# Performance work log

Measured on AMD Instinct MI355X. Metric: run time of the kernel, lower is better.

The kernel has to match this reference:

```python
import jax, jax.numpy as jnp
import numpy as np

EPS = 1e-5
SLOPE = 0.2
DIMS = [128, 32, 64, 32, 16, 8, 4, 2]  # widths before final Linear(2,1)


def _layernorm(h, g, b):
    m = jnp.mean(h, axis=-1, keepdims=True)
    v = jnp.mean(jnp.square(h - m), axis=-1, keepdims=True)
    return (h - m) * jax.lax.rsqrt(v + EPS) * g + b


def setup_inputs() -> dict:
    key = jax.random.key(0)
    ks = jax.random.split(key, 2 * len(DIMS) + 2)
    inp = {"x": jax.random.normal(ks[0], (524288, DIMS[0]), dtype=jnp.float32)}
    # 7 bias-free Linears, each followed by LayerNorm(gamma, beta)
    for i in range(7):
        din, dout = DIMS[i], DIMS[i + 1]
        inp[f"W{i+1}"] = jax.random.normal(ks[2 * i + 1], (din, dout), dtype=jnp.float32) / np.sqrt(din)
        inp[f"g{i+1}"] = jnp.ones((dout,), dtype=jnp.float32)
        inp[f"bt{i+1}"] = jnp.zeros((dout,), dtype=jnp.float32)
    # final Linear(2 -> 1) with bias
    inp["W8"] = jax.random.normal(ks[-1], (2, 1), dtype=jnp.float32) / np.sqrt(2.0)
    inp["b8"] = jnp.zeros((1,), dtype=jnp.float32)
    return inp


def reference(x, W1, g1, bt1, W2, g2, bt2, W3, g3, bt3, W4, g4, bt4,
              W5, g5, bt5, W6, g6, bt6, W7, g7, bt7, W8, b8):
    Ws = [W1, W2, W3, W4, W5, W6, W7]
    gs = [g1, g2, g3, g4, g5, g6, g7]
    bs = [bt1, bt2, bt3, bt4, bt5, bt6, bt7]
    h = x
    for W, g, b in zip(Ws, gs, bs):
        h = jnp.dot(h, W)                 # Linear, bias=False
        h = _layernorm(h, g, b)           # LayerNorm
        h = jnp.where(h > 0, h, SLOPE * h)  # LeakyReLU(0.2)
    return jnp.dot(h, W8) + b8            # final Linear(2, 1)
```

## Files before the change

kernel.cpp:

```cpp
#include <hip/hip_runtime.h>

#define EPS 1e-5f
#define SLOPE 0.2f

typedef float v2f __attribute__((ext_vector_type(2)));

__device__ __forceinline__ v2f pkfma(float s, v2f w, v2f a) {
  v2f sv = {s, s};
  return __builtin_elementwise_fma(sv, w, a);
}

template<int N2>
__device__ __forceinline__ void ln_lrelu_pk(v2f* h, const float* __restrict__ g,
                                            const float* __restrict__ b) {
  const v2f* g2 = reinterpret_cast<const v2f*>(g);
  const v2f* b2 = reinterpret_cast<const v2f*>(b);
  const float invN = 1.0f / (2 * N2);
  float m, vv;
  if constexpr (N2 >= 2) {
    v2f s0 = {0.f, 0.f}, s1 = {0.f, 0.f};
#pragma unroll
    for (int j = 0; j < N2; j += 2) { s0 += h[j]; s1 += h[j + 1]; }
    v2f st = s0 + s1;
    m = (st.x + st.y) * invN;
    v2f q0 = {0.f, 0.f}, q1 = {0.f, 0.f};
#pragma unroll
    for (int j = 0; j < N2; j += 2) {
      v2f d0 = h[j] - m, d1 = h[j + 1] - m;
      q0 = __builtin_elementwise_fma(d0, d0, q0);
      q1 = __builtin_elementwise_fma(d1, d1, q1);
    }
    v2f qt = q0 + q1;
    vv = (qt.x + qt.y) * invN;
  } else {
    m = (h[0].x + h[0].y) * 0.5f;
    float dx = h[0].x - m, dy = h[0].y - m;
    vv = (dx * dx + dy * dy) * 0.5f;
  }
  const float rs = rsqrtf(vv + EPS);
#pragma unroll
  for (int j = 0; j < N2; ++j) {
    v2f t = (h[j] - m) * rs * g2[j] + b2[j];
    h[j] = __builtin_elementwise_max(t, SLOPE * t);
  }
}

template<int DIN, int DOUT2>
__device__ __forceinline__ void linear_pk(const v2f* hin, v2f* hout,
                                          const float* __restrict__ W) {
#pragma unroll
  for (int j = 0; j < DOUT2; ++j) hout[j] = (v2f){0.f, 0.f};
#pragma unroll
  for (int k = 0; k < DIN; ++k) {
    float hk = (k & 1) ? hin[k >> 1].y : hin[k >> 1].x;
    const v2f* wr = reinterpret_cast<const v2f*>(W + k * (DOUT2 * 2));
#pragma unroll
    for (int j = 0; j < DOUT2; ++j) hout[j] = pkfma(hk, wr[j], hout[j]);
  }
}

__global__ __launch_bounds__(256) void disc_fused(
    const float* __restrict__ x,
    const float* __restrict__ W1, const float* __restrict__ g1, const float* __restrict__ b1,
    const float* __restrict__ W2, const float* __restrict__ g2, const float* __restrict__ b2,
    const float* __restrict__ W3, const float* __restrict__ g3, const float* __restrict__ b3,
    const float* __restrict__ W4, const float* __restrict__ g4, const float* __restrict__ b4,
    const float* __restrict__ W5, const float* __restrict__ g5, const float* __restrict__ b5,
    const float* __restrict__ W6, const float* __restrict__ g6, const float* __restrict__ b6,
    const float* __restrict__ W7, const float* __restrict__ g7, const float* __restrict__ b7,
    const float* __restrict__ W8, const float* __restrict__ b8,
    float* __restrict__ out, int nrows) {
  const long row = (long)blockIdx.x * 256 + threadIdx.x;
  if (row >= (long)nrows) return;

  const float4* __restrict__ xr4 = reinterpret_cast<const float4*>(x) + row * 32;
  v2f h1[16];
#pragma unroll
  for (int j = 0; j < 16; ++j) h1[j] = (v2f){0.f, 0.f};

#pragma unroll 1
  for (int cc = 0; cc < 4; ++cc) {
    float4 bv[8];
#pragma unroll
    for (int q = 0; q < 8; ++q) bv[q] = xr4[cc * 8 + q];
#pragma unroll
    for (int q = 0; q < 8; ++q) {
#pragma unroll
      for (int kk = 0; kk < 4; ++kk) {
        float xk = (kk == 0) ? bv[q].x : (kk == 1) ? bv[q].y
                 : (kk == 2) ? bv[q].z : bv[q].w;
        const v2f* wr =
            reinterpret_cast<const v2f*>(W1 + (cc * 32 + q * 4 + kk) * 32);
#pragma unroll
        for (int j = 0; j < 16; ++j) h1[j] = pkfma(xk, wr[j], h1[j]);
      }
    }
  }
  ln_lrelu_pk<16>(h1, g1, b1);

  const v2f* W2v = reinterpret_cast<const v2f*>(W2);

  float sum2 = 0.f, sq2 = 0.f;
#pragma unroll 1
  for (int jb = 0; jb < 16; ++jb) {
    v2f a01 = {0.f, 0.f}, a23 = {0.f, 0.f};
#pragma unroll
    for (int k = 0; k < 32; ++k) {
      float hk = (k & 1) ? h1[k >> 1].y : h1[k >> 1].x;
      a01 = pkfma(hk, W2v[k * 32 + jb * 2], a01);
      a23 = pkfma(hk, W2v[k * 32 + jb * 2 + 1], a23);
    }
    sum2 += (a01.x + a01.y) + (a23.x + a23.y);
    sq2 = fmaf(a01.x, a01.x, sq2); sq2 = fmaf(a01.y, a01.y, sq2);
    sq2 = fmaf(a23.x, a23.x, sq2); sq2 = fmaf(a23.y, a23.y, sq2);
  }
  const float m2 = sum2 * (1.0f / 64.0f);
  const float v2 = fmaf(-m2, m2, sq2 * (1.0f / 64.0f));
  const float rs2 = rsqrtf(v2 + EPS);

  v2f h3[16];
#pragma unroll
  for (int i = 0; i < 16; ++i) h3[i] = (v2f){0.f, 0.f};
#pragma unroll 1
  for (int jb = 0; jb < 16; ++jb) {
    v2f a01 = {0.f, 0.f}, a23 = {0.f, 0.f};
#pragma unroll
    for (int k = 0; k < 32; ++k) {
      float hk = (k & 1) ? h1[k >> 1].y : h1[k >> 1].x;
      a01 = pkfma(hk, W2v[k * 32 + jb * 2], a01);
      a23 = pkfma(hk, W2v[k * 32 + jb * 2 + 1], a23);
    }
#pragma unroll
    for (int u = 0; u < 4; ++u) {
      float a = (u == 0) ? a01.x : (u == 1) ? a01.y : (u == 2) ? a23.x : a23.y;
      int j = jb * 4 + u;
      float y = (a - m2) * rs2 * g2[j] + b2[j];
      y = fmaxf(y, SLOPE * y);
      const v2f* wr3 = reinterpret_cast<const v2f*>(W3 + j * 32);
#pragma unroll
      for (int i = 0; i < 16; ++i) h3[i] = pkfma(y, wr3[i], h3[i]);
    }
  }
  ln_lrelu_pk<16>(h3, g3, b3);

  v2f h4[8]; linear_pk<32, 8>(h3, h4, W4); ln_lrelu_pk<8>(h4, g4, b4);
  v2f h5[4]; linear_pk<16, 4>(h4, h5, W5); ln_lrelu_pk<4>(h5, g5, b5);
  v2f h6[2]; linear_pk<8, 2>(h5, h6, W6);  ln_lrelu_pk<2>(h6, g6, b6);
  v2f h7[1]; linear_pk<4, 1>(h6, h7, W7);  ln_lrelu_pk<1>(h7, g7, b7);

  out[row] = fmaf(h7[0].y, W8[1], fmaf(h7[0].x, W8[0], b8[0]));
}

extern "C" void kernel_launch(void* const* d_in, const int* in_sizes, int n_in,
                              void* d_out, int out_size, void* d_ws, size_t ws_size,
                              hipStream_t stream) {
  const float* x  = (const float*)d_in[0];
  const float* W1 = (const float*)d_in[1];
  const float* g1 = (const float*)d_in[2];
  const float* b1 = (const float*)d_in[3];
  const float* W2 = (const float*)d_in[4];
  const float* g2 = (const float*)d_in[5];
  const float* b2 = (const float*)d_in[6];
  const float* W3 = (const float*)d_in[7];
  const float* g3 = (const float*)d_in[8];
  const float* b3 = (const float*)d_in[9];
  const float* W4 = (const float*)d_in[10];
  const float* g4 = (const float*)d_in[11];
  const float* b4 = (const float*)d_in[12];
  const float* W5 = (const float*)d_in[13];
  const float* g5 = (const float*)d_in[14];
  const float* b5 = (const float*)d_in[15];
  const float* W6 = (const float*)d_in[16];
  const float* g6 = (const float*)d_in[17];
  const float* b6 = (const float*)d_in[18];
  const float* W7 = (const float*)d_in[19];
  const float* g7 = (const float*)d_in[20];
  const float* b7 = (const float*)d_in[21];
  const float* W8 = (const float*)d_in[22];
  const float* b8 = (const float*)d_in[23];
  float* out = (float*)d_out;

  const int nrows = in_sizes[0] / 128;
  const int grid = (nrows + 255) / 256;
  hipLaunchKernelGGL(disc_fused, dim3(grid), dim3(256), 0, stream,
                     x, W1, g1, b1, W2, g2, b2, W3, g3, b3, W4, g4, b4,
                     W5, g5, b5, W6, g6, b6, W7, g7, b7, W8, b8, out, nrows);
}
```

Before: 151.9 us.

## Process two rows per thread to amortize weight loads across rows

Each thread now computes two consecutive rows, sharing every weight load between two sets of packed FMAs across all layers, and the grid is halved. A dummy 44KB shared-memory array caps occupancy so the doubled register footprint fits without spilling. The intent is to cut weight-load and instruction overhead per row. The cost is higher register pressure, fewer resident waves to hide memory latency, and less coalesced x reads because rows are strided by two per thread.

```diff
diff --git a/kernel.cpp b/kernel.cpp
--- a/kernel.cpp
+++ b/kernel.cpp
@@ -11,51 +11,73 @@
 }
 
 template<int N2>
-__device__ __forceinline__ void ln_lrelu_pk(v2f* h, const float* __restrict__ g,
-                                            const float* __restrict__ b) {
+__device__ __forceinline__ void ln_lrelu_pk2(v2f* __restrict__ ha, v2f* __restrict__ hb,
+                                             const float* __restrict__ g,
+                                             const float* __restrict__ b) {
   const v2f* g2 = reinterpret_cast<const v2f*>(g);
   const v2f* b2 = reinterpret_cast<const v2f*>(b);
   const float invN = 1.0f / (2 * N2);
-  float m, vv;
+  float ma, mb, va, vb;
   if constexpr (N2 >= 2) {
-    v2f s0 = {0.f, 0.f}, s1 = {0.f, 0.f};
-#pragma unroll
-    for (int j = 0; j < N2; j += 2) { s0 += h[j]; s1 += h[j + 1]; }
-    v2f st = s0 + s1;
-    m = (st.x + st.y) * invN;
-    v2f q0 = {0.f, 0.f}, q1 = {0.f, 0.f};
+    v2f sa0 = {0.f, 0.f}, sa1 = {0.f, 0.f}, sb0 = {0.f, 0.f}, sb1 = {0.f, 0.f};
 #pragma unroll
     for (int j = 0; j < N2; j += 2) {
-      v2f d0 = h[j] - m, d1 = h[j + 1] - m;
-      q0 = __builtin_elementwise_fma(d0, d0, q0);
-      q1 = __builtin_elementwise_fma(d1, d1, q1);
-    }
-    v2f qt = q0 + q1;
-    vv = (qt.x + qt.y) * invN;
+      sa0 += ha[j]; sa1 += ha[j + 1];
+      sb0 += hb[j]; sb1 += hb[j + 1];
+    }
+    v2f sat = sa0 + sa1, sbt = sb0 + sb1;
+    ma = (sat.x + sat.y) * invN;
+    mb = (sbt.x + sbt.y) * invN;
+    v2f qa0 = {0.f, 0.f}, qa1 = {0.f, 0.f}, qb0 = {0.f, 0.f}, qb1 = {0.f, 0.f};
+#pragma unroll
+    for (int j = 0; j < N2; j += 2) {
+      v2f da0 = ha[j] - ma, da1 = ha[j + 1] - ma;
+      v2f db0 = hb[j] - mb, db1 = hb[j + 1] - mb;
+      qa0 = __builtin_elementwise_fma(da0, da0, qa0);
+      qa1 = __builtin_elementwise_fma(da1, da1, qa1);
+      qb0 = __builtin_elementwise_fma(db0, db0, qb0);
+      qb1 = __builtin_elementwise_fma(db1, db1, qb1);
+    }
+    v2f qat = qa0 + qa1, qbt = qb0 + qb1;
+    va = (qat.x + qat.y) * invN;
+    vb = (qbt.x + qbt.y) * invN;
   } else {
-    m = (h[0].x + h[0].y) * 0.5f;
-    float dx = h[0].x - m, dy = h[0].y - m;
-    vv = (dx * dx + dy * dy) * 0.5f;
-  }
-  const float rs = rsqrtf(vv + EPS);
+    ma = (ha[0].x + ha[0].y) * 0.5f;
+    mb = (hb[0].x + hb[0].y) * 0.5f;
+    float dax = ha[0].x - ma, day = ha[0].y - ma;
+    float dbx = hb[0].x - mb, dby = hb[0].y - mb;
+    va = (dax * dax + day * day) * 0.5f;
+    vb = (dbx * dbx + dby * dby) * 0.5f;
+  }
+  const float rsa = rsqrtf(va + EPS);
+  const float rsb = rsqrtf(vb + EPS);
 #pragma unroll
   for (int j = 0; j < N2; ++j) {
-    v2f t = (h[j] - m) * rs * g2[j] + b2[j];
-    h[j] = __builtin_elementwise_max(t, SLOPE * t);
+    v2f gj = g2[j], bj = b2[j];
+    v2f ta = (ha[j] - ma) * rsa * gj + bj;
+    v2f tb = (hb[j] - mb) * rsb * gj + bj;
+    ha[j] = __builtin_elementwise_max(ta, SLOPE * ta);
+    hb[j] = __builtin_elementwise_max(tb, SLOPE * tb);
   }
 }
 
 template<int DIN, int DOUT2>
-__device__ __forceinline__ void linear_pk(const v2f* hin, v2f* hout,
-                                          const float* __restrict__ W) {
-#pragma unroll
-  for (int j = 0; j < DOUT2; ++j) hout[j] = (v2f){0.f, 0.f};
+__device__ __forceinline__ void linear_pk2(const v2f* ha, const v2f* hb,
+                                           v2f* oa, v2f* ob,
+                                           const float* __restrict__ W) {
+#pragma unroll
+  for (int j = 0; j < DOUT2; ++j) { oa[j] = (v2f){0.f, 0.f}; ob[j] = (v2f){0.f, 0.f}; }
 #pragma unroll
   for (int k = 0; k < DIN; ++k) {
-    float hk = (k & 1) ? hin[k >> 1].y : hin[k >> 1].x;
+    float xa = (k & 1) ? ha[k >> 1].y : ha[k >> 1].x;
+    float xb = (k & 1) ? hb[k >> 1].y : hb[k >> 1].x;
     const v2f* wr = reinterpret_cast<const v2f*>(W + k * (DOUT2 * 2));
 #pragma unroll
-    for (int j = 0; j < DOUT2; ++j) hout[j] = pkfma(hk, wr[j], hout[j]);
+    for (int j = 0; j < DOUT2; ++j) {
+      v2f w = wr[j];
+      oa[j] = pkfma(xa, w, oa[j]);
+      ob[j] = pkfma(xb, w, ob[j]);
+    }
   }
 }
 
@@ -70,85 +92,126 @@
     const float* __restrict__ W7, const float* __restrict__ g7, const float* __restrict__ b7,
     const float* __restrict__ W8, const float* __restrict__ b8,
     float* __restrict__ out, int nrows) {
-  const long row = (long)blockIdx.x * 256 + threadIdx.x;
-  if (row >= (long)nrows) return;
-
-  const float4* __restrict__ xr4 = reinterpret_cast<const float4*>(x) + row * 32;
-  v2f h1[16];
-#pragma unroll
-  for (int j = 0; j < 16; ++j) h1[j] = (v2f){0.f, 0.f};
+  __shared__ float ldspad[11264];
+  if (threadIdx.x == 0) *(volatile float*)&ldspad[0] = 0.f;
+
+  const int tid = threadIdx.x;
+  const long ra = (long)blockIdx.x * 512 + 2 * (long)tid;
+  if (ra >= (long)nrows) return;
+  long rb = ra + 1;
+  const bool bok = rb < (long)nrows;
+  if (!bok) rb = ra;
+
+  const float4* __restrict__ xa4 = reinterpret_cast<const float4*>(x) + ra * 32;
+  const float4* __restrict__ xb4 = reinterpret_cast<const float4*>(x) + rb * 32;
+
+  v2f h1a[16], h1b[16];
+#pragma unroll
+  for (int j = 0; j < 16; ++j) { h1a[j] = (v2f){0.f, 0.f}; h1b[j] = (v2f){0.f, 0.f}; }
 
 #pragma unroll 1
   for (int cc = 0; cc < 4; ++cc) {
-    float4 bv[8];
-#pragma unroll
-    for (int q = 0; q < 8; ++q) bv[q] = xr4[cc * 8 + q];
+    float4 A[8], B[8];
+#pragma unroll
+    for (int q = 0; q < 8; ++q) A[q] = xa4[cc * 8 + q];
+#pragma unroll
+    for (int q = 0; q < 8; ++q) B[q] = xb4[cc * 8 + q];
 #pragma unroll
     for (int q = 0; q < 8; ++q) {
 #pragma unroll
       for (int kk = 0; kk < 4; ++kk) {
-        float xk = (kk == 0) ? bv[q].x : (kk == 1) ? bv[q].y
-                 : (kk == 2) ? bv[q].z : bv[q].w;
+        float xka = (kk == 0) ? A[q].x : (kk == 1) ? A[q].y
+                  : (kk == 2) ? A[q].z : A[q].w;
+        float xkb = (kk == 0) ? B[q].x : (kk == 1) ? B[q].y
+                  : (kk == 2) ? B[q].z : B[q].w;
         const v2f* wr =
             reinterpret_cast<const v2f*>(W1 + (cc * 32 + q * 4 + kk) * 32);
 #pragma unroll
-        for (int j = 0; j < 16; ++j) h1[j] = pkfma(xk, wr[j], h1[j]);
+        for (int j = 0; j < 16; ++j) {
+          v2f w = wr[j];
+          h1a[j] = pkfma(xka, w, h1a[j]);
+          h1b[j] = pkfma(xkb, w, h1b[j]);
+        }
       }
     }
   }
-  ln_lrelu_pk<16>(h1, g1, b1);
+  ln_lrelu_pk2<16>(h1a, h1b, g1, b1);
 
   const v2f* W2v = reinterpret_cast<const v2f*>(W2);
 
-  float sum2 = 0.f, sq2 = 0.f;
+  float suma = 0.f, sqa = 0.f, sumb = 0.f, sqb = 0.f;
 #pragma unroll 1
   for (int jb = 0; jb < 16; ++jb) {
-    v2f a01 = {0.f, 0.f}, a23 = {0.f, 0.f};
+    v2f a01 = {0.f, 0.f}, a23 = {0.f, 0.f}, c01 = {0.f, 0.f}, c23 = {0.f, 0.f};
 #pragma unroll
     for (int k = 0; k < 32; ++k) {
-      float hk = (k & 1) ? h1[k >> 1].y : h1[k >> 1].x;
-      a01 = pkfma(hk, W2v[k * 32 + jb * 2], a01);
-      a23 = pkfma(hk, W2v[k * 32 + jb * 2 + 1], a23);
-    }
-    sum2 += (a01.x + a01.y) + (a23.x + a23.y);
-    sq2 = fmaf(a01.x, a01.x, sq2); sq2 = fmaf(a01.y, a01.y, sq2);
-    sq2 = fmaf(a23.x, a23.x, sq2); sq2 = fmaf(a23.y, a23.y, sq2);
-  }
-  const float m2 = sum2 * (1.0f / 64.0f);
-  const float v2 = fmaf(-m2, m2, sq2 * (1.0f / 64.0f));
-  const float rs2 = rsqrtf(v2 + EPS);
-
-  v2f h3[16];
-#pragma unroll
-  for (int i = 0; i < 16; ++i) h3[i] = (v2f){0.f, 0.f};
+      float xa = (k & 1) ? h1a[k >> 1].y : h1a[k >> 1].x;
+      float xb = (k & 1) ? h1b[k >> 1].y : h1b[k >> 1].x;
+      v2f w01 = W2v[k * 32 + jb * 2], w23 = W2v[k * 32 + jb * 2 + 1];
+      a01 = pkfma(xa, w01, a01); a23 = pkfma(xa, w23, a23);
+      c01 = pkfma(xb, w01, c01); c23 = pkfma(xb, w23, c23);
+    }
+    suma += (a01.x + a01.y) + (a23.x + a23.y);
+    sqa = fmaf(a01.x, a01.x, sqa); sqa = fmaf(a01.y, a01.y, sqa);
+    sqa = fmaf(a23.x, a23.x, sqa); sqa = fmaf(a23.y, a23.y, sqa);
+    sumb += (c01.x + c01.y) + (c23.x + c23.y);
+    sqb = fmaf(c01.x, c01.x, sqb); sqb = fmaf(c01.y, c01.y, sqb);
+    sqb = fmaf(c23.x, c23.x, sqb); sqb = fmaf(c23.y, c23.y, sqb);
+  }
+  const float m2a = suma * (1.0f / 64.0f);
+  const float v2a = fmaf(-m2a, m2a, sqa * (1.0f / 64.0f));
+  const float rs2a = rsqrtf(v2a + EPS);
+  const float m2b = sumb * (1.0f / 64.0f);
+  const float v2b = fmaf(-m2b, m2b, sqb * (1.0f / 64.0f));
+  const float rs2b = rsqrtf(v2b + EPS);
+
+  v2f h3a[16], h3b[16];
+#pragma unroll
+  for (int i = 0; i < 16; ++i) { h3a[i] = (v2f){0.f, 0.f}; h3b[i] = (v2f){0.f, 0.f}; }
 #pragma unroll 1
   for (int jb = 0; jb < 16; ++jb) {
-    v2f a01 = {0.f, 0.f}, a23 = {0.f, 0.f};
+    v2f a01 = {0.f, 0.f}, a23 = {0.f, 0.f}, c01 = {0.f, 0.f}, c23 = {0.f, 0.f};
 #pragma unroll
     for (int k = 0; k < 32; ++k) {
-      float hk = (k & 1) ? h1[k >> 1].y : h1[k >> 1].x;
-      a01 = pkfma(hk, W2v[k * 32 + jb * 2], a01);
-      a23 = pkfma(hk, W2v[k * 32 + jb * 2 + 1], a23);
+      float xa = (k & 1) ? h1a[k >> 1].y : h1a[k >> 1].x;
+      float xb = (k & 1) ? h1b[k >> 1].y : h1b[k >> 1].x;
+      v2f w01 = W2v[k * 32 + jb * 2], w23 = W2v[k * 32 + jb * 2 + 1];
+      a01 = pkfma(xa, w01, a01); a23 = pkfma(xa, w23, a23);
+      c01 = pkfma(xb, w01, c01); c23 = pkfma(xb, w23, c23);
     }
 #pragma unroll
     for (int u = 0; u < 4; ++u) {
-      float a = (u == 0) ? a01.x : (u == 1) ? a01.y : (u == 2) ? a23.x : a23.y;
+      float av = (u == 0) ? a01.x : (u == 1) ? a01.y : (u == 2) ? a23.x : a23.y;
+      float cv = (u == 0) ? c01.x : (u == 1) ? c01.y : (u == 2) ? c23.x : c23.y;
       int j = jb * 4 + u;
-      float y = (a - m2) * rs2 * g2[j] + b2[j];
-      y = fmaxf(y, SLOPE * y);
+      float gj = g2[j], bj = b2[j];
+      float ya = (av - m2a) * rs2a * gj + bj;
+      float yb = (cv - m2b) * rs2b * gj + bj;
+      ya = fmaxf(ya, SLOPE * ya);
+      yb = fmaxf(yb, SLOPE * yb);
       const v2f* wr3 = reinterpret_cast<const v2f*>(W3 + j * 32);
 #pragma unroll
-      for (int i = 0; i < 16; ++i) h3[i] = pkfma(y, wr3[i], h3[i]);
-    }
-  }
-  ln_lrelu_pk<16>(h3, g3, b3);
-
-  v2f h4[8]; linear_pk<32, 8>(h3, h4, W4); ln_lrelu_pk<8>(h4, g4, b4);
-  v2f h5[4]; linear_pk<16, 4>(h4, h5, W5); ln_lrelu_pk<4>(h5, g5, b5);
-  v2f h6[2]; linear_pk<8, 2>(h5, h6, W6);  ln_lrelu_pk<2>(h6, g6, b6);
-  v2f h7[1]; linear_pk<4, 1>(h6, h7, W7);  ln_lrelu_pk<1>(h7, g7, b7);
-
-  out[row] = fmaf(h7[0].y, W8[1], fmaf(h7[0].x, W8[0], b8[0]));
+      for (int i = 0; i < 16; ++i) {
+        v2f w = wr3[i];
+        h3a[i] = pkfma(ya, w, h3a[i]);
+        h3b[i] = pkfma(yb, w, h3b[i]);
+      }
+    }
+  }
+  ln_lrelu_pk2<16>(h3a, h3b, g3, b3);
+
+  v2f h4a[8], h4b[8];
+  linear_pk2<32, 8>(h3a, h3b, h4a, h4b, W4); ln_lrelu_pk2<8>(h4a, h4b, g4, b4);
+  v2f h5a[4], h5b[4];
+  linear_pk2<16, 4>(h4a, h4b, h5a, h5b, W5); ln_lrelu_pk2<4>(h5a, h5b, g5, b5);
+  v2f h6a[2], h6b[2];
+  linear_pk2<8, 2>(h5a, h5b, h6a, h6b, W6);  ln_lrelu_pk2<2>(h6a, h6b, g6, b6);
+  v2f h7a[1], h7b[1];
+  linear_pk2<4, 1>(h6a, h6b, h7a, h7b, W7);  ln_lrelu_pk2<1>(h7a, h7b, g7, b7);
+
+  const float w80 = W8[0], w81 = W8[1], bb8 = b8[0];
+  out[ra] = fmaf(h7a[0].y, w81, fmaf(h7a[0].x, w80, bb8));
+  if (bok) out[rb] = fmaf(h7b[0].y, w81, fmaf(h7b[0].x, w80, bb8));
 }
 
 extern "C" void kernel_launch(void* const* d_in, const int* in_sizes, int n_in,
@@ -181,7 +244,7 @@
   float* out = (float*)d_out;
 
   const int nrows = in_sizes[0] / 128;
-  const int grid = (nrows + 255) / 256;
+  const int grid = (nrows + 511) / 512;
   hipLaunchKernelGGL(disc_fused, dim3(grid), dim3(256), 0, stream,
                      x, W1, g1, b1, W2, g2, b2, W3, g3, b3, W4, g4, b4,
                      W5, g5, b5, W6, g6, b6, W7, g7, b7, W8, b8, out, nrows);
```

Result: slower. 176.3 us (+16.0%).

## Compute layer-2 LayerNorm statistics via precomputed Gram matrix of W2

Applied to the files above, without the earlier changes.

Adds a small setup kernel that computes W2·W2ᵀ (32x32) and the row sums of W2 into the workspace. The main kernel then gets the layer-2 mean as a dot product and the second moment as a quadratic form in h1. This replaces the first full 64-wide layer-2 matmul pass used only for statistics, halving that pass's FMA count. It adds an extra kernel launch and changes the rounding of the variance computation.

```diff
diff --git a/kernel.cpp b/kernel.cpp
--- a/kernel.cpp
+++ b/kernel.cpp
@@ -56,6 +56,27 @@
     const v2f* wr = reinterpret_cast<const v2f*>(W + k * (DOUT2 * 2));
 #pragma unroll
     for (int j = 0; j < DOUT2; ++j) hout[j] = pkfma(hk, wr[j], hout[j]);
+  }
+}
+
+__global__ __launch_bounds__(256) void setup_gram(const float* __restrict__ W2,
+                                                  float* __restrict__ ws) {
+  const int t = threadIdx.x;
+  for (int e = t; e < 1024; e += 256) {
+    const int k = e >> 5, kp = e & 31;
+    const float* __restrict__ a = W2 + k * 64;
+    const float* __restrict__ b = W2 + kp * 64;
+    float s = 0.f;
+#pragma unroll
+    for (int j = 0; j < 64; ++j) s = fmaf(a[j], b[j], s);
+    ws[e] = s;
+  }
+  if (t < 32) {
+    const float* __restrict__ a = W2 + t * 64;
+    float s = 0.f;
+#pragma unroll
+    for (int j = 0; j < 64; ++j) s += a[j];
+    ws[1024 + t] = s;
   }
 }
 
@@ -69,6 +90,7 @@
     const float* __restrict__ W6, const float* __restrict__ g6, const float* __restrict__ b6,
     const float* __restrict__ W7, const float* __restrict__ g7, const float* __restrict__ b7,
     const float* __restrict__ W8, const float* __restrict__ b8,
+    const float* __restrict__ ws,
     float* __restrict__ out, int nrows) {
   const long row = (long)blockIdx.x * 256 + threadIdx.x;
   if (row >= (long)nrows) return;
@@ -98,26 +120,33 @@
   }
   ln_lrelu_pk<16>(h1, g1, b1);
 
-  const v2f* W2v = reinterpret_cast<const v2f*>(W2);
-
-  float sum2 = 0.f, sq2 = 0.f;
+  const v2f* Qv = reinterpret_cast<const v2f*>(ws);
+  const v2f* Cv = reinterpret_cast<const v2f*>(ws + 1024);
+
+  v2f macc = {0.f, 0.f};
+#pragma unroll
+  for (int k2 = 0; k2 < 16; ++k2)
+    macc = __builtin_elementwise_fma(h1[k2], Cv[k2], macc);
+  const float m2 = (macc.x + macc.y) * (1.0f / 64.0f);
+
+  v2f qacc = {0.f, 0.f};
 #pragma unroll 1
-  for (int jb = 0; jb < 16; ++jb) {
-    v2f a01 = {0.f, 0.f}, a23 = {0.f, 0.f};
+  for (int kb = 0; kb < 8; ++kb) {
+    v2f t01 = {0.f, 0.f}, t23 = {0.f, 0.f};
 #pragma unroll
     for (int k = 0; k < 32; ++k) {
       float hk = (k & 1) ? h1[k >> 1].y : h1[k >> 1].x;
-      a01 = pkfma(hk, W2v[k * 32 + jb * 2], a01);
-      a23 = pkfma(hk, W2v[k * 32 + jb * 2 + 1], a23);
-    }
-    sum2 += (a01.x + a01.y) + (a23.x + a23.y);
-    sq2 = fmaf(a01.x, a01.x, sq2); sq2 = fmaf(a01.y, a01.y, sq2);
-    sq2 = fmaf(a23.x, a23.x, sq2); sq2 = fmaf(a23.y, a23.y, sq2);
-  }
-  const float m2 = sum2 * (1.0f / 64.0f);
-  const float v2 = fmaf(-m2, m2, sq2 * (1.0f / 64.0f));
+      t01 = pkfma(hk, Qv[k * 16 + kb * 2], t01);
+      t23 = pkfma(hk, Qv[k * 16 + kb * 2 + 1], t23);
+    }
+    qacc = __builtin_elementwise_fma(t01, h1[kb * 2], qacc);
+    qacc = __builtin_elementwise_fma(t23, h1[kb * 2 + 1], qacc);
+  }
+  const float E2 = (qacc.x + qacc.y) * (1.0f / 64.0f);
+  const float v2 = fmaf(-m2, m2, E2);
   const float rs2 = rsqrtf(v2 + EPS);
 
+  const v2f* W2v = reinterpret_cast<const v2f*>(W2);
   v2f h3[16];
 #pragma unroll
   for (int i = 0; i < 16; ++i) h3[i] = (v2f){0.f, 0.f};
@@ -179,10 +208,13 @@
   const float* W8 = (const float*)d_in[22];
   const float* b8 = (const float*)d_in[23];
   float* out = (float*)d_out;
+  float* ws = (float*)d_ws;
 
   const int nrows = in_sizes[0] / 128;
   const int grid = (nrows + 255) / 256;
+
+  hipLaunchKernelGGL(setup_gram, dim3(1), dim3(256), 0, stream, W2, ws);
   hipLaunchKernelGGL(disc_fused, dim3(grid), dim3(256), 0, stream,
                      x, W1, g1, b1, W2, g2, b2, W3, g3, b3, W4, g4, b4,
-                     W5, g5, b5, W6, g6, b6, W7, g7, b7, W8, b8, out, nrows);
-}
+                     W5, g5, b5, W6, g6, b6, W7, g7, b7, W8, b8, ws, out, nrows);
+}
```

Result: slower. 159.0 us (+4.7%).
